# Kernel optimization log

Hardware: AMD Instinct MI355X
Metric: run time of the kernel (lower is better)

Reference implementation:

```python
import jax, jax.numpy as jnp
import numpy as np
from jax import lax

N_WIRES = 4
EPS_BN = 1e-5

def _conv(x, w, b):
    y = lax.conv_general_dilated(x, w, (1, 1), 'SAME',
                                 dimension_numbers=('NCHW', 'OIHW', 'NCHW'))
    return y + b[None, :, None, None]

def _bn2d(x, g, b):
    mu = jnp.mean(x, axis=(0, 2, 3), keepdims=True)
    var = jnp.var(x, axis=(0, 2, 3), keepdims=True)
    return (x - mu) * lax.rsqrt(var + EPS_BN) * g[None, :, None, None] + b[None, :, None, None]

def _maxpool2(x):
    return lax.reduce_window(x, -jnp.inf, lax.max, (1, 1, 2, 2), (1, 1, 2, 2), 'VALID')

def _ry(t):
    c, s = jnp.cos(t / 2), jnp.sin(t / 2)
    return jnp.stack([jnp.stack([c, -s], -1), jnp.stack([s, c], -1)], -2).astype(jnp.complex64)

def _rz(t):
    tc = t.astype(jnp.complex64)
    em, ep = jnp.exp(-0.5j * tc), jnp.exp(0.5j * tc)
    z = jnp.zeros_like(em)
    return jnp.stack([jnpp_stack := jnp.stack([em, z], -1), jnp.stack([z, ep], -1)], -2)

def _rx(t):
    c = jnp.cos(t / 2).astype(jnp.complex64)
    s = (-1j) * jnp.sin(t / 2).astype(jnp.complex64)
    return jnp.stack([jnp.stack([c, s], -1), jnp.stack([s, c], -1)], -2)

def _apply_1q(state, U, q):
    # state: (B,2,2,2,2); U: (2,2) shared or (B,2,2) per-sample
    a = jnp.moveaxis(state, 1 + q, 1)
    if U.ndim == 2:
        a = jnp.einsum('ij,bj...->bi...', U, a)
    else:
        a = jnp.einsum('bij,bj...->bi...', U, a)
    return jnp.moveaxis(a, 1, 1 + q)

def _cnot(state, c, t):
    a = jnp.moveaxis(state, (1 + c, 1 + t), (1, 2))
    a = jnp.stack([a[:, 0], jnp.flip(a[:, 1], axis=1)], axis=1)
    return jnp.moveaxis(a, (1, 2), (1 + c, 1 + t))

def _circuit(scaled, theta, rho):
    # scaled: (B, 4) angles; theta, rho: (4, 3)
    B = scaled.shape[0]
    state = jnp.zeros((B,) + (2,) * N_WIRES, jnp.complex64)
    state = state.at[(slice(None),) + (0,) * N_WIRES].set(1.0 + 0j)
    for i in range(N_WIRES):
        state = _apply_1q(state, _ry(scaled[:, i]), i)
    for i in range(N_WIRES):
        state = _apply_1q(state, _ry(theta[i, 0]), i)
        state = _apply_1q(state, _rz(theta[i, 1]), i)
        state = _apply_1q(state, _rx(theta[i, 2]), i)
    for i in range(N_WIRES - 1):
        state = _cnot(state, i, i + 1)
    for i in range(N_WIRES):
        state = _apply_1q(state, _ry(rho[i, 0]), i)
        state = _apply_1q(state, _rz(rho[i, 1]), i)
        state = _apply_1q(state, _rx(rho[i, 2]), i)
    for i in range(N_WIRES - 1):
        state = _cnot(state, i + 1, i)
    probs = jnp.abs(state) ** 2  # (B,2,2,2,2)
    exps = []
    for i in range(N_WIRES):
        p = jnp.moveaxis(probs, 1 + i, 1)
        exps.append(jnp.sum(p[:, 0], axis=(1, 2, 3)) - jnp.sum(p[:, 1], axis=(1, 2, 3)))
    return jnp.stack(exps, axis=1)  # (B,4)

def setup_inputs() -> dict:
    key = jax.random.key(0)
    ks = jax.random.split(key, 8)
    B = 128
    return {
        'x': jax.random.normal(ks[0], (B, 1, 224, 224), jnp.float32),
        'conv1_w': jax.random.normal(ks[1], (8, 1, 3, 3), jnp.float32) * 0.1,
        'conv1_b': jnp.zeros((8,), jnp.float32),
        'bn1_g': jnp.ones((8,), jnp.float32),
        'bn1_b': jnp.zeros((8,), jnp.float32),
        'conv2_w': jax.random.normal(ks[2], (16, 8, 3, 3), jnp.float32) * 0.1,
        'conv2_b': jnp.zeros((16,), jnp.float32),
        'bn2_g': jnp.ones((16,), jnp.float32),
        'bn2_b': jnp.zeros((16,), jnp.float32),
        'theta': jax.random.normal(ks[3], (4, 3), jnp.float32),
        'rho': jax.random.normal(ks[4], (4, 3), jnp.float32),
        'norm_g': jnp.ones((4,), jnp.float32),
        'norm_b': jnp.zeros((4,), jnp.float32),
    }

def reference(x, conv1_w, conv1_b, bn1_g, bn1_b, conv2_w, conv2_b, bn2_g, bn2_b,
              theta, rho, norm_g, norm_b):
    h = jax.nn.relu(_bn2d(_conv(x, conv1_w, conv1_b), bn1_g, bn1_b))
    h = _maxpool2(h)
    h = jax.nn.relu(_bn2d(_conv(h, conv2_w, conv2_b), bn2_g, bn2_b))
    h = _maxpool2(h)
    feat = jnp.mean(h, axis=(2, 3))          # AdaptiveAvgPool2d((1,1)) + flatten -> (B,16)
    feat = feat[:, :N_WIRES]                  # (B,4)
    scaled = (feat - jnp.mean(feat)) / (jnp.std(feat, ddof=1) + 1e-6) * jnp.pi
    out = _circuit(scaled, theta, rho)        # (B,4) real
    mu = jnp.mean(out, axis=0, keepdims=True)
    var = jnp.var(out, axis=0, keepdims=True)
    return (out - mu) * lax.rsqrt(var + EPS_BN) * norm_g[None, :] + norm_b[None, :]
```

## Files before the change

### kernel.cpp

```cpp
#include <hip/hip_runtime.h>
#include <math.h>

#define H1 224
#define W1 224
#define H2 112
#define W2 112
#define HP 56
#define WP 56

#define NS 32
#define SLOT_STRIDE 64

struct C2 { float re, im; };
__device__ __forceinline__ C2 cmul(C2 a, C2 b) {
    return C2{fmaf(a.re, b.re, -a.im * b.im), fmaf(a.re, b.im, a.im * b.re)};
}
__device__ __forceinline__ C2 cadd(C2 a, C2 b) { return C2{a.re + b.re, a.im + b.im}; }

template <int S>
__device__ __forceinline__ void ap1s(C2* st, C2 u00, C2 u01, C2 u10, C2 u11) {
#pragma unroll
    for (int i = 0; i < 16; i++) {
        if (i & S) continue;
        C2 a0 = st[i], a1 = st[i + S];
        st[i]     = cadd(cmul(u00, a0), cmul(u01, a1));
        st[i + S] = cadd(cmul(u10, a0), cmul(u11, a1));
    }
}
template <int SC, int STT>
__device__ __forceinline__ void cnot_s(C2* st) {
#pragma unroll
    for (int i = 0; i < 16; i++)
        if ((i & SC) && !(i & STT)) { C2 t = st[i]; st[i] = st[i + STT]; st[i + STT] = t; }
}
struct M2 { C2 m[2][2]; };
__device__ __forceinline__ M2 mmul(const M2& A, const M2& B) {
    M2 R;
#pragma unroll
    for (int i = 0; i < 2; i++)
#pragma unroll
        for (int j = 0; j < 2; j++)
            R.m[i][j] = cadd(cmul(A.m[i][0], B.m[0][j]), cmul(A.m[i][1], B.m[1][j]));
    return R;
}
__device__ __forceinline__ M2 combined_u(const float* __restrict__ p) {
    float c0 = cosf(0.5f * p[0]), s0 = sinf(0.5f * p[0]);
    float c1 = cosf(0.5f * p[1]), s1 = sinf(0.5f * p[1]);
    float c2 = cosf(0.5f * p[2]), s2 = sinf(0.5f * p[2]);
    M2 Ry = {{{{c0, 0.f}, {-s0, 0.f}}, {{s0, 0.f}, {c0, 0.f}}}};
    M2 Rz = {{{{c1, -s1}, {0.f, 0.f}}, {{0.f, 0.f}, {c1, s1}}}};
    M2 Rx = {{{{c2, 0.f}, {0.f, -s2}}, {{0.f, -s2}, {c2, 0.f}}}};
    return mmul(Rx, mmul(Rz, Ry));
}

template <int Q>
__device__ __forceinline__ void rows_reduce(float* red, const float* vals, int tid) {
#pragma unroll
    for (int q = 0; q < Q; q++) red[q * 256 + tid] = vals[q];
    __syncthreads();
#pragma unroll
    for (int s = 128; s > 0; s >>= 1) {
        for (int idx = tid; idx < Q * s; idx += 256) {
            int row = idx / s, i = idx - row * s;
            red[row * 256 + i] += red[row * 256 + i + s];
        }
        __syncthreads();
    }
}

__global__ void zero_ws(float* ws, int n) {
    int i = blockIdx.x * blockDim.x + threadIdx.x;
    if (i < n) ws[i] = 0.f;
}

__device__ __forceinline__ float slot_sum(const float* stats, int c) {
    float s = 0.f;
#pragma unroll
    for (int sl = 0; sl < NS; sl++) s += stats[sl * SLOT_STRIDE + c];
    return s;
}

__global__ __launch_bounds__(256, 2) void conv1_pool_stats(
        const float* __restrict__ x, const float* __restrict__ w,
        const float* __restrict__ bias, const float* __restrict__ g1,
        float* __restrict__ stats, float* __restrict__ p1ext) {
    __shared__ float red[16 * 256];
    int strip = blockIdx.x;
    int b = blockIdx.y;
    int tid = threadIdx.x;
    int pc = tid & 127;
    int rhalf = tid >> 7;
    int r0 = strip * 16 + rhalf * 8;
    const float* xb = x + (size_t)b * H1 * W1;
    float sums[8], sqs[8], pm[8];
    bool gp[8];
#pragma unroll
    for (int c = 0; c < 8; c++) { sums[c] = 0.f; sqs[c] = 0.f; gp[c] = g1[c] >= 0.f; }
    bool act = pc < W2;
    if (act) {
        bool cl = pc > 0, cr = pc < W2 - 1;
        const float* rp0 = xb + (size_t)r0 * W1 + 2 * pc;
        float al, am0, am1, ar, bl, bm0, bm1, br;
        if (r0 > 0) {
            const float* rp = rp0 - W1;
            float2 m = *(const float2*)rp;
            al = cl ? rp[-1] : 0.f; am0 = m.x; am1 = m.y; ar = cr ? rp[2] : 0.f;
        } else { al = 0.f; am0 = 0.f; am1 = 0.f; ar = 0.f; }
        {
            float2 m = *(const float2*)rp0;
            bl = cl ? rp0[-1] : 0.f; bm0 = m.x; bm1 = m.y; br = cr ? rp0[2] : 0.f;
        }
#pragma unroll
        for (int rr = 0; rr < 8; rr++) {
            float nl = 0.f, nm0 = 0.f, nm1 = 0.f, nr = 0.f;
            int rn = r0 + rr + 1;
            if (rn < H1) {
                const float* rp = rp0 + (size_t)(rr + 1) * W1;
                float2 m = *(const float2*)rp;
                nl = cl ? rp[-1] : 0.f; nm0 = m.x; nm1 = m.y; nr = cr ? rp[2] : 0.f;
            }
            float4 e0 = make_float4(0.f, 0.f, 0.f, 0.f);
            float4 e1 = make_float4(0.f, 0.f, 0.f, 0.f);
#pragma unroll
            for (int c = 0; c < 8; c++) {
                const float* wc = w + c * 9;
                float y0 = bias[c], y1 = bias[c];
                y0 = fmaf(wc[0], al,  y0); y0 = fmaf(wc[1], am0, y0); y0 = fmaf(wc[2], am1, y0);
                y1 = fmaf(wc[0], am0, y1); y1 = fmaf(wc[1], am1, y1); y1 = fmaf(wc[2], ar,  y1);
                y0 = fmaf(wc[3], bl,  y0); y0 = fmaf(wc[4], bm0, y0); y0 = fmaf(wc[5], bm1, y0);
                y1 = fmaf(wc[3], bm0, y1); y1 = fmaf(wc[4], bm1, y1); y1 = fmaf(wc[5], br,  y1);
                y0 = fmaf(wc[6], nl,  y0); y0 = fmaf(wc[7], nm0, y0); y0 = fmaf(wc[8], nm1, y0);
                y1 = fmaf(wc[6], nm0, y1); y1 = fmaf(wc[7], nm1, y1); y1 = fmaf(wc[8], nr,  y1);
                sums[c] += y0 + y1;
                sqs[c] = fmaf(y0, y0, fmaf(y1, y1, sqs[c]));
                float m01 = gp[c] ? fmaxf(y0, y1) : fminf(y0, y1);
                if ((rr & 1) == 0) {
                    pm[c] = m01;
                } else {
                    float e = gp[c] ? fmaxf(pm[c], m01) : fminf(pm[c], m01);
                    if (c == 0) e0.x = e; else if (c == 1) e0.y = e;
                    else if (c == 2) e0.z = e; else if (c == 3) e0.w = e;
                    else if (c == 4) e1.x = e; else if (c == 5) e1.y = e;
                    else if (c == 6) e1.z = e; else e1.w = e;
                }
            }
            if (rr & 1) {
                int pr = (r0 + rr) >> 1;
                float* dst = p1ext + ((((size_t)b * H2 + pr) * W2 + pc) << 3);
                ((float4*)dst)[0] = e0;
                ((float4*)dst)[1] = e1;
            }
            al = bl; am0 = bm0; am1 = bm1; ar = br;
            bl = nl; bm0 = nm0; bm1 = nm1; br = nr;
        }
    }
    float vals[16];
#pragma unroll
    for (int c = 0; c < 8; c++) { vals[c] = sums[c]; vals[8 + c] = sqs[c]; }
    rows_reduce<16>(red, vals, tid);
    int slot = (b * 14 + strip) & (NS - 1);
    if (tid < 16) atomicAdd(stats + slot * SLOT_STRIDE + tid, red[tid * 256]);
}

__global__ void conv1_stats(const float* __restrict__ x, const float* __restrict__ w,
                            const float* __restrict__ bias, float* __restrict__ stats) {
    __shared__ float red[16 * 256];
    int strip = blockIdx.x;
    int b = blockIdx.y;
    int tid = threadIdx.x;
    const float* xb = x + (size_t)b * H1 * W1;
    float sums[8], sqs[8];
#pragma unroll
    for (int c = 0; c < 8; c++) { sums[c] = 0.f; sqs[c] = 0.f; }
    int col = tid;
    if (col < W1) {
        bool cl = col > 0, cr = col < W1 - 1;
        int row0 = strip * 8;
        float a0, a1, a2, b0, b1, b2, c0, c1, c2;
        {
            int r = row0 - 1;
            if (r >= 0) {
                a0 = cl ? xb[r * W1 + col - 1] : 0.f;
                a1 = xb[r * W1 + col];
                a2 = cr ? xb[r * W1 + col + 1] : 0.f;
            } else { a0 = a1 = a2 = 0.f; }
            r = row0;
            b0 = cl ? xb[r * W1 + col - 1] : 0.f;
            b1 = xb[r * W1 + col];
            b2 = cr ? xb[r * W1 + col + 1] : 0.f;
        }
        for (int rr = 0; rr < 8; rr++) {
            int rn = row0 + rr + 1;
            if (rn < H1) {
                c0 = cl ? xb[rn * W1 + col - 1] : 0.f;
                c1 = xb[rn * W1 + col];
                c2 = cr ? xb[rn * W1 + col + 1] : 0.f;
            } else { c0 = c1 = c2 = 0.f; }
#pragma unroll
            for (int c = 0; c < 8; c++) {
                float acc = bias[c];
                acc = fmaf(w[c * 9 + 0], a0, acc);
                acc = fmaf(w[c * 9 + 1], a1, acc);
                acc = fmaf(w[c * 9 + 2], a2, acc);
                acc = fmaf(w[c * 9 + 3], b0, acc);
                acc = fmaf(w[c * 9 + 4], b1, acc);
                acc = fmaf(w[c * 9 + 5], b2, acc);
                acc = fmaf(w[c * 9 + 6], c0, acc);
                acc = fmaf(w[c * 9 + 7], c1, acc);
                acc = fmaf(w[c * 9 + 8], c2, acc);
                sums[c] += acc;
                sqs[c] = fmaf(acc, acc, sqs[c]);
            }
            a0 = b0; a1 = b1; a2 = b2;
            b0 = c0; b1 = c1; b2 = c2;
        }
    }
    float vals[16];
#pragma unroll
    for (int c = 0; c < 8; c++) { vals[c] = sums[c]; vals[8 + c] = sqs[c]; }
    rows_reduce<16>(red, vals, tid);
    int slot = (b * 28 + strip) & (NS - 1);
    if (tid < 16) atomicAdd(stats + slot * SLOT_STRIDE + tid, red[tid * 256]);
}

template <int PH, int PW>
__device__ __forceinline__ void build_h1_tile(const float* __restrict__ xb,
                                              float (*h1t)[PH][PW],
                                              const float* __restrict__ w1,
                                              const float* __restrict__ b1,
                                              const float* sc1, const float* sh1,
                                              int oy0, int ox0, int tid) {
    for (int i = tid; i < PH * PW; i += 256) {
        int p = i / PW, q = i % PW;
        int hy = oy0 + p, hx = ox0 + q;
        bool ok = (hy >= 0 && hy < H2 && hx >= 0 && hx < W2);
        float xp[5][5];
        if (hy >= 1 && hy <= H2 - 2 && hx >= 1 && hx <= W2 - 2) {
            const float* bp = xb + (2 * hy - 1) * W1 + (2 * hx - 1);
#pragma unroll
            for (int r = 0; r < 5; r++)
#pragma unroll
                for (int c = 0; c < 5; c++) xp[r][c] = bp[r * W1 + c];
        } else if (ok) {
#pragma unroll
            for (int r = 0; r < 5; r++)
#pragma unroll
                for (int c = 0; c < 5; c++) {
                    int gy = 2 * hy - 1 + r, gx = 2 * hx - 1 + c;
                    xp[r][c] = (gy >= 0 && gy < H1 && gx >= 0 && gx < W1) ? xb[gy * W1 + gx] : 0.f;
                }
        }
#pragma unroll
        for (int c = 0; c < 8; c++) {
            float mx = 0.f;
            if (ok) {
                mx = -INFINITY;
#pragma unroll
                for (int dy = 0; dy < 2; dy++)
#pragma unroll
                    for (int dx = 0; dx < 2; dx++) {
                        float acc = b1[c];
#pragma unroll
                        for (int ky = 0; ky < 3; ky++)
#pragma unroll
                            for (int kx = 0; kx < 3; kx++)
                                acc = fmaf(w1[c * 9 + ky * 3 + kx], xp[dy + ky][dx + kx], acc);
                        mx = fmaxf(mx, fmaxf(fmaf(acc, sc1[c], sh1[c]), 0.f));
                    }
            }
            h1t[c][p][q] = mx;
        }
    }
}

__global__ __launch_bounds__(256, 4) void conv2_stats_slim(
        const float* __restrict__ p1ext, const float* __restrict__ g1,
        const float* __restrict__ be1, const float* __restrict__ stats1,
        const float* __restrict__ w2, const float* __restrict__ b2,
        const float* __restrict__ g2,
        float* __restrict__ stats2, float* __restrict__ p2ext, float N1) {
    __shared__ __align__(16) float h1t[8][34][34];
    __shared__ float sc1[8], sh1[8];
    int b = blockIdx.z;
    int Y0 = blockIdx.y * 32, X0 = blockIdx.x * 32;
    int ty = threadIdx.y, tx = threadIdx.x;
    int tid = ty * 16 + tx;
    if (tid < 8) {
        float su = slot_sum(stats1, tid), sq = slot_sum(stats1, 8 + tid);
        float mu = su / N1;
        float var = sq / N1 - mu * mu;
        float sc = g1[tid] * rsqrtf(var + 1e-5f);
        sc1[tid] = sc;
        sh1[tid] = be1[tid] - mu * sc;
    }
    __syncthreads();
    const float* pb = p1ext + (((size_t)b * H2) * W2 << 3);
    for (int i = tid; i < 34 * 34; i += 256) {
        int p = i / 34, q = i % 34;
        int hy = Y0 - 1 + p, hx = X0 - 1 + q;
        if (hy >= 0 && hy < H2 && hx >= 0 && hx < W2) {
            const float* cp = pb + (((size_t)hy * W2 + hx) << 3);
            float4 u = ((const float4*)cp)[0];
            float4 v = ((const float4*)cp)[1];
            h1t[0][p][q] = fmaxf(fmaf(u.x, sc1[0], sh1[0]), 0.f);
            h1t[1][p][q] = fmaxf(fmaf(u.y, sc1[1], sh1[1]), 0.f);
            h1t[2][p][q] = fmaxf(fmaf(u.z, sc1[2], sh1[2]), 0.f);
            h1t[3][p][q] = fmaxf(fmaf(u.w, sc1[3], sh1[3]), 0.f);
            h1t[4][p][q] = fmaxf(fmaf(v.x, sc1[4], sh1[4]), 0.f);
            h1t[5][p][q] = fmaxf(fmaf(v.y, sc1[5], sh1[5]), 0.f);
            h1t[6][p][q] = fmaxf(fmaf(v.z, sc1[6], sh1[6]), 0.f);
            h1t[7][p][q] = fmaxf(fmaf(v.w, sc1[7], sh1[7]), 0.f);
        } else {
#pragma unroll
            for (int c = 0; c < 8; c++) h1t[c][p][q] = 0.f;
        }
    }
    __syncthreads();
    float acc[4][2][2];
#pragma unroll
    for (int co = 0; co < 4; co++)
#pragma unroll
        for (int dy = 0; dy < 2; dy++)
#pragma unroll
            for (int dx = 0; dx < 2; dx++) acc[co][dy][dx] = b2[co];
#pragma unroll
    for (int ci = 0; ci < 8; ci++) {
        float win[4][4];
#pragma unroll
        for (int r = 0; r < 4; r++) {
            const float2* rp = (const float2*)&h1t[ci][2 * ty + r][2 * tx];
            float2 u = rp[0], v = rp[1];
            win[r][0] = u.x; win[r][1] = u.y; win[r][2] = v.x; win[r][3] = v.y;
        }
#pragma unroll
        for (int co = 0; co < 4; co++)
#pragma unroll
            for (int ky = 0; ky < 3; ky++)
#pragma unroll
                for (int kx = 0; kx < 3; kx++) {
                    float wv = w2[co * 72 + ci * 9 + ky * 3 + kx];
#pragma unroll
                    for (int dy = 0; dy < 2; dy++)
#pragma unroll
                        for (int dx = 0; dx < 2; dx++)
                            acc[co][dy][dx] = fmaf(wv, win[dy + ky][dx + kx], acc[co][dy][dx]);
                }
    }
    int cy0 = Y0 + 2 * ty, cx0 = X0 + 2 * tx;
    bool vy0 = cy0 < H2, vy1 = cy0 + 1 < H2, vx0 = cx0 < W2, vx1 = cx0 + 1 < W2;
    float vals[8];
#pragma unroll
    for (int co = 0; co < 4; co++) {
        float s = 0.f, q = 0.f;
        if (vy0 && vx0) { float a = acc[co][0][0]; s += a; q = fmaf(a, a, q); }
        if (vy0 && vx1) { float a = acc[co][0][1]; s += a; q = fmaf(a, a, q); }
        if (vy1 && vx0) { float a = acc[co][1][0]; s += a; q = fmaf(a, a, q); }
        if (vy1 && vx1) { float a = acc[co][1][1]; s += a; q = fmaf(a, a, q); }
        vals[co] = s;
        vals[4 + co] = q;
    }
    {
        int hy = (Y0 >> 1) + ty, hx = (X0 >> 1) + tx;
        if (hy < HP && hx < WP) {
#pragma unroll
            for (int co = 0; co < 4; co++) {
                float mx = fmaxf(fmaxf(acc[co][0][0], acc[co][0][1]),
                                 fmaxf(acc[co][1][0], acc[co][1][1]));
                float mn = fminf(fminf(acc[co][0][0], acc[co][0][1]),
                                 fminf(acc[co][1][0], acc[co][1][1]));
                p2ext[(((size_t)b * 4 + co) * HP + hy) * WP + hx] = (g2[co] >= 0.f) ? mx : mn;
            }
        }
    }
    __syncthreads();
    float* red = (float*)h1t;
    rows_reduce<8>(red, vals, tid);
    int slot = ((b * 16) + blockIdx.y * 4 + blockIdx.x) & (NS - 1);
    if (tid < 8) atomicAdd(stats2 + slot * SLOT_STRIDE + tid, red[tid * 256]);
}

template <bool STORE>
__global__ __launch_bounds__(256, 4) void conv2_stats_fused(
        const float* __restrict__ x, const float* __restrict__ w1,
        const float* __restrict__ b1, const float* __restrict__ g1,
        const float* __restrict__ be1, const float* __restrict__ stats1,
        const float* __restrict__ w2, const float* __restrict__ b2,
        float* __restrict__ stats2,
        float* __restrict__ pmax, float* __restrict__ pmin, float N1) {
    __shared__ __align__(16) float h1t[8][34][34];
    __shared__ float sc1[8], sh1[8];
    int b = blockIdx.z;
    int Y0 = blockIdx.y * 32, X0 = blockIdx.x * 32;
    int ty = threadIdx.y, tx = threadIdx.x;
    int tid = ty * 16 + tx;
    if (tid < 8) {
        float su = slot_sum(stats1, tid), sq = slot_sum(stats1, 8 + tid);
        float mu = su / N1;
        float var = sq / N1 - mu * mu;
        float sc = g1[tid] * rsqrtf(var + 1e-5f);
        sc1[tid] = sc;
        sh1[tid] = be1[tid] - mu * sc;
    }
    __syncthreads();
    const float* xb = x + (size_t)b * H1 * W1;
    build_h1_tile<34, 34>(xb, h1t, w1, b1, sc1, sh1, Y0 - 1, X0 - 1, tid);
    __syncthreads();
    float acc[4][2][2];
#pragma unroll
    for (int co = 0; co < 4; co++)
#pragma unroll
        for (int dy = 0; dy < 2; dy++)
#pragma unroll
            for (int dx = 0; dx < 2; dx++) acc[co][dy][dx] = b2[co];
#pragma unroll
    for (int ci = 0; ci < 8; ci++) {
        float win[4][4];
#pragma unroll
        for (int r = 0; r < 4; r++) {
            const float2* rp = (const float2*)&h1t[ci][2 * ty + r][2 * tx];
            float2 u = rp[0], v = rp[1];
            win[r][0] = u.x; win[r][1] = u.y; win[r][2] = v.x; win[r][3] = v.y;
        }
#pragma unroll
        for (int co = 0; co < 4; co++)
#pragma unroll
            for (int ky = 0; ky < 3; ky++)
#pragma unroll
                for (int kx = 0; kx < 3; kx++) {
                    float wv = w2[co * 72 + ci * 9 + ky * 3 + kx];
#pragma unroll
                    for (int dy = 0; dy < 2; dy++)
#pragma unroll
                        for (int dx = 0; dx < 2; dx++)
                            acc[co][dy][dx] = fmaf(wv, win[dy + ky][dx + kx], acc[co][dy][dx]);
                }
    }
    int cy0 = Y0 + 2 * ty, cx0 = X0 + 2 * tx;
    bool vy0 = cy0 < H2, vy1 = cy0 + 1 < H2, vx0 = cx0 < W2, vx1 = cx0 + 1 < W2;
    float vals[8];
#pragma unroll
    for (int co = 0; co < 4; co++) {
        float s = 0.f, q = 0.f;
        if (vy0 && vx0) { float a = acc[co][0][0]; s += a; q = fmaf(a, a, q); }
        if (vy0 && vx1) { float a = acc[co][0][1]; s += a; q = fmaf(a, a, q); }
        if (vy1 && vx0) { float a = acc[co][1][0]; s += a; q = fmaf(a, a, q); }
        if (vy1 && vx1) { float a = acc[co][1][1]; s += a; q = fmaf(a, a, q); }
        vals[co] = s;
        vals[4 + co] = q;
    }
    if (STORE) {
        int hy = (Y0 >> 1) + ty, hx = (X0 >> 1) + tx;
        if (hy < HP && hx < WP) {
#pragma unroll
            for (int co = 0; co < 4; co++) {
                float mx = fmaxf(fmaxf(acc[co][0][0], acc[co][0][1]),
                                 fmaxf(acc[co][1][0], acc[co][1][1]));
                float mn = fminf(fminf(acc[co][0][0], acc[co][0][1]),
                                 fminf(acc[co][1][0], acc[co][1][1]));
                size_t idx = (((size_t)b * 4 + co) * HP + hy) * WP + hx;
                pmax[idx] = mx;
                pmin[idx] = mn;
            }
        }
    }
    __syncthreads();
    float* red = (float*)h1t;
    rows_reduce<8>(red, vals, tid);
    int slot = ((b * 16) + blockIdx.y * 4 + blockIdx.x) & (NS - 1);
    if (tid < 8) atomicAdd(stats2 + slot * SLOT_STRIDE + tid, red[tid * 256]);
}

__global__ void pool_bn_mean(const float* __restrict__ pmax, const float* __restrict__ pmin,
                             const float* __restrict__ g2, const float* __restrict__ be2,
                             const float* __restrict__ stats2,
                             float* __restrict__ featbuf, float N2) {
    __shared__ float red[256];
    int co = blockIdx.x & 3;
    int b = blockIdx.x >> 2;
    int tid = threadIdx.x;
    float su = slot_sum(stats2, co), sq = slot_sum(stats2, 4 + co);
    float mu = su / N2;
    float var = sq / N2 - mu * mu;
    float sc = g2[co] * rsqrtf(var + 1e-5f);
    float sh = be2[co] - mu * sc;
    const float* P = (sc >= 0.f ? pmax : pmin) + ((size_t)b * 4 + co) * (HP * WP);
    float s = 0.f;
    for (int i = tid; i < HP * WP; i += 256) s += fmaxf(fmaf(P[i], sc, sh), 0.f);
    red[tid] = s;
    __syncthreads();
    for (int st = 128; st > 0; st >>= 1) {
        if (tid < st) red[tid] += red[tid + st];
        __syncthreads();
    }
    if (tid == 0) featbuf[(size_t)b * 4 + co] = red[0];
}

__global__ void conv2_final_fused(const float* __restrict__ x, const float* __restrict__ w1,
                                  const float* __restrict__ b1, const float* __restrict__ g1,
                                  const float* __restrict__ be1,
                                  const float* __restrict__ stats1,
                                  const float* __restrict__ w2, const float* __restrict__ b2,
                                  const float* __restrict__ g2, const float* __restrict__ be2,
                                  const float* __restrict__ stats2,
                                  float* __restrict__ featbuf, float N1, float N2) {
    __shared__ __align__(16) float h1t[8][34][34];
    __shared__ float sc1[8], sh1[8];
    __shared__ float sc2[4], sh2[4];
    int b = blockIdx.z;
    int py0 = blockIdx.y * 16, px0 = blockIdx.x * 16;
    int ty = threadIdx.y, tx = threadIdx.x;
    int tid = ty * 16 + tx;
    if (tid < 8) {
        float su = slot_sum(stats1, tid), sq = slot_sum(stats1, 8 + tid);
        float mu = su / N1;
        float var = sq / N1 - mu * mu;
        float sc = g1[tid] * rsqrtf(var + 1e-5f);
        sc1[tid] = sc;
        sh1[tid] = be1[tid] - mu * sc;
    }
    if (tid >= 16 && tid < 20) {
        int j = tid - 16;
        float su = slot_sum(stats2, j), sq = slot_sum(stats2, 4 + j);
        float mu = su / N2;
        float var = sq / N2 - mu * mu;
        float sc = g2[j] * rsqrtf(var + 1e-5f);
        sc2[j] = sc;
        sh2[j] = be2[j] - mu * sc;
    }
    __syncthreads();
    const float* xb = x + (size_t)b * H1 * W1;
    build_h1_tile<34, 34>(xb, h1t, w1, b1, sc1, sh1, 2 * py0 - 1, 2 * px0 - 1, tid);
    __syncthreads();
    bool valid = (py0 + ty < HP) && (px0 + tx < WP);
    float acc[4][2][2];
#pragma unroll
    for (int co = 0; co < 4; co++)
#pragma unroll
        for (int dy = 0; dy < 2; dy++)
#pragma unroll
            for (int dx = 0; dx < 2; dx++) acc[co][dy][dx] = b2[co];
#pragma unroll
    for (int ci = 0; ci < 8; ci++) {
        float win[4][4];
#pragma unroll
        for (int r = 0; r < 4; r++) {
            const float2* rp = (const float2*)&h1t[ci][2 * ty + r][2 * tx];
            float2 u = rp[0], v = rp[1];
            win[r][0] = u.x; win[r][1] = u.y; win[r][2] = v.x; win[r][3] = v.y;
        }
#pragma unroll
        for (int co = 0; co < 4; co++)
#pragma unroll
            for (int ky = 0; ky < 3; ky++)
#pragma unroll
                for (int kx = 0; kx < 3; kx++) {
                    float wv = w2[co * 72 + ci * 9 + ky * 3 + kx];
#pragma unroll
                    for (int dy = 0; dy < 2; dy++)
#pragma unroll
                        for (int dx = 0; dx < 2; dx++)
                            acc[co][dy][dx] = fmaf(wv, win[dy + ky][dx + kx], acc[co][dy][dx]);
                }
    }
    float vals[4];
#pragma unroll
    for (int co = 0; co < 4; co++) {
        float mx = -INFINITY;
#pragma unroll
        for (int dy = 0; dy < 2; dy++)
#pragma unroll
            for (int dx = 0; dx < 2; dx++)
                mx = fmaxf(mx, fmaxf(fmaf(acc[co][dy][dx], sc2[co], sh2[co]), 0.f));
        vals[co] = valid ? mx : 0.f;
    }
    __syncthreads();
    float* red = (float*)h1t;
    rows_reduce<4>(red, vals, tid);
    if (tid < 4) atomicAdd(featbuf + (size_t)b * 4 + tid, red[tid * 256]);
}

__device__ __forceinline__ float bsum(float v, float* lds) {
#pragma unroll
    for (int off = 32; off; off >>= 1) v += __shfl_xor(v, off, 64);
    __syncthreads();
    if ((threadIdx.x & 63) == 0) lds[threadIdx.x >> 6] = v;
    __syncthreads();
    float r = 0.f;
    int nw = (int)(blockDim.x + 63) >> 6;
#pragma clang loop unroll(disable)
    for (int i = 0; i < nw; i++) r += lds[i];
    return r;
}

__global__ void finalize(const float* __restrict__ featbuf, const float* __restrict__ theta,
                         const float* __restrict__ rho, const float* __restrict__ ng,
                         const float* __restrict__ nb, float* __restrict__ out, int B) {
    __shared__ float lds[16];
    int b = threadIdx.x;
    float f[4];
#pragma unroll
    for (int j = 0; j < 4; j++) f[j] = featbuf[b * 4 + j] * (1.f / (HP * WP));
    float n = 4.f * (float)B;
    float mean = bsum(f[0] + f[1] + f[2] + f[3], lds) / n;
    float d2 = 0.f;
#pragma unroll
    for (int j = 0; j < 4; j++) { float d = f[j] - mean; d2 += d * d; }
    float var1 = bsum(d2, lds) / (n - 1.f);
    float stdv = sqrtf(fmaxf(var1, 0.f)) + 1e-6f;
    const float PI = 3.14159265358979323846f;
    float cs[4], sn[4];
#pragma unroll
    for (int j = 0; j < 4; j++) {
        float sc = (f[j] - mean) / stdv * PI;
        cs[j] = cosf(0.5f * sc);
        sn[j] = sinf(0.5f * sc);
    }
    C2 st[16];
    {
        float amp[16];
        amp[1] = sn[3]; amp[0] = cs[3];
#pragma unroll
        for (int k = 0; k < 2; k++) { amp[k + 2] = amp[k] * sn[2]; amp[k] *= cs[2]; }
#pragma unroll
        for (int k = 0; k < 4; k++) { amp[k + 4] = amp[k] * sn[1]; amp[k] *= cs[1]; }
#pragma unroll
        for (int k = 0; k < 8; k++) { amp[k + 8] = amp[k] * sn[0]; amp[k] *= cs[0]; }
#pragma unroll
        for (int i = 0; i < 16; i++) st[i] = C2{amp[i], 0.f};
    }
#pragma clang loop unroll(disable)
    for (int l = 0; l < 2; l++) {
        const float* p = (l == 0) ? theta : rho;
#pragma clang loop unroll(disable)
        for (int i = 0; i < 4; i++) {
            M2 U = combined_u(p + i * 3);
            switch (i) {
            case 0: ap1s<8>(st, U.m[0][0], U.m[0][1], U.m[1][0], U.m[1][1]); break;
            case 1: ap1s<4>(st, U.m[0][0], U.m[0][1], U.m[1][0], U.m[1][1]); break;
            case 2: ap1s<2>(st, U.m[0][0], U.m[0][1], U.m[1][0], U.m[1][1]); break;
            default: ap1s<1>(st, U.m[0][0], U.m[0][1], U.m[1][0], U.m[1][1]); break;
            }
        }
        if (l == 0) { cnot_s<8, 4>(st); cnot_s<4, 2>(st); cnot_s<2, 1>(st); }
        else        { cnot_s<4, 8>(st); cnot_s<2, 4>(st); cnot_s<1, 2>(st); }
    }
    float e[4];
#pragma unroll
    for (int qb = 0; qb < 4; qb++) {
        int m = 8 >> qb;
        float p0 = 0.f, p1 = 0.f;
#pragma unroll
        for (int i = 0; i < 16; i++) {
            float pr = st[i].re * st[i].re + st[i].im * st[i].im;
            if (i & m) p1 += pr; else p0 += pr;
        }
        e[qb] = p0 - p1;
    }
#pragma clang loop unroll(disable)
    for (int j = 0; j < 4; j++) {
        float mu = bsum(e[j], lds) / (float)B;
        float dv = e[j] - mu;
        float v = bsum(dv * dv, lds) / (float)B;
        out[b * 4 + j] = fmaf(dv, rsqrtf(v + 1e-5f) * ng[j], nb[j]);
    }
}

extern "C" void kernel_launch(void* const* d_in, const int* in_sizes, int n_in,
                              void* d_out, int out_size, void* d_ws, size_t ws_size,
                              hipStream_t stream) {
    const float* x     = (const float*)d_in[0];
    const float* w1    = (const float*)d_in[1];
    const float* b1    = (const float*)d_in[2];
    const float* g1    = (const float*)d_in[3];
    const float* be1   = (const float*)d_in[4];
    const float* w2    = (const float*)d_in[5];
    const float* b2    = (const float*)d_in[6];
    const float* g2    = (const float*)d_in[7];
    const float* be2   = (const float*)d_in[8];
    const float* theta = (const float*)d_in[9];
    const float* rho   = (const float*)d_in[10];
    const float* ng    = (const float*)d_in[11];
    const float* nb    = (const float*)d_in[12];
    float* out = (float*)d_out;

    int B = in_sizes[0] / (H1 * W1);

    float* ws = (float*)d_ws;
    float* stats1 = ws;
    float* stats2 = ws + NS * SLOT_STRIDE;
    float* featbuf = ws + 2 * NS * SLOT_STRIDE;
    float* bufs = featbuf + (size_t)B * 4;

    size_t common = (size_t)(2 * NS * SLOT_STRIDE) + (size_t)B * 4;
    size_t p2n = (size_t)B * 4 * HP * WP;
    size_t p1n = (size_t)B * 8 * H2 * W2;
    size_t needA = (common + p2n + p1n) * sizeof(float);
    size_t needB = (common + 2 * p2n) * sizeof(float);
    bool tierA = ws_size >= needA;
    bool tierB = !tierA && ws_size >= needB;

    float N1 = (float)B * H1 * W1;
    float N2 = (float)B * H2 * W2;
    int nz = (int)common;

    zero_ws<<<(nz + 255) / 256, 256, 0, stream>>>(ws, nz);
    if (tierA) {
        float* p2ext = bufs;
        float* p1ext = bufs + p2n;
        conv1_pool_stats<<<dim3(14, B), 256, 0, stream>>>(x, w1, b1, g1, stats1, p1ext);
        conv2_stats_slim<<<dim3(4, 4, B), dim3(16, 16), 0, stream>>>(
            p1ext, g1, be1, stats1, w2, b2, g2, stats2, p2ext, N1);
        pool_bn_mean<<<B * 4, 256, 0, stream>>>(p2ext, p2ext, g2, be2, stats2, featbuf, N2);
        finalize<<<1, B, 0, stream>>>(featbuf, theta, rho, ng, nb, out, B);
    } else if (tierB) {
        float* pmax = bufs;
        float* pmin = bufs + p2n;
        conv1_stats<<<dim3(28, B), 256, 0, stream>>>(x, w1, b1, stats1);
        conv2_stats_fused<true><<<dim3(4, 4, B), dim3(16, 16), 0, stream>>>(
            x, w1, b1, g1, be1, stats1, w2, b2, stats2, pmax, pmin, N1);
        pool_bn_mean<<<B * 4, 256, 0, stream>>>(pmax, pmin, g2, be2, stats2, featbuf, N2);
        finalize<<<1, B, 0, stream>>>(featbuf, theta, rho, ng, nb, out, B);
    } else {
        conv1_stats<<<dim3(28, B), 256, 0, stream>>>(x, w1, b1, stats1);
        conv2_stats_fused<false><<<dim3(4, 4, B), dim3(16, 16), 0, stream>>>(
            x, w1, b1, g1, be1, stats1, w2, b2, stats2, nullptr, nullptr, N1);
        conv2_final_fused<<<dim3(4, 4, B), dim3(16, 16), 0, stream>>>(
            x, w1, b1, g1, be1, stats1, w2, b2, g2, be2, stats2, featbuf, N1, N2);
        finalize<<<1, B, 0, stream>>>(featbuf, theta, rho, ng, nb, out, B);
    }
}
```

Baseline: 170.3 us.

## Replace shared-memory tiled conv2 with direct per-thread global-load strip kernel

The conv2 stage no longer stages a 34x34x8 BN+ReLU halo tile in LDS. Each thread now computes one pooled output column over two pooled rows, reading its 4x4 input window straight from global memory with float4 loads and applying BN1+ReLU in registers. The launch becomes a 1D grid of 7 blocks per sample, and the two __syncthreads around the LDS tile are gone. In exchange, overlapping windows are loaded redundantly from global or cache instead of being shared through LDS, register pressure rises from the 4x4x4 window array, and a no-op zero add is inserted in mmul.

```diff
diff --git a/kernel.cpp b/kernel.cpp
--- a/kernel.cpp
+++ b/kernel.cpp
@@ -40,7 +40,7 @@
     for (int i = 0; i < 2; i++)
 #pragma unroll
         for (int j = 0; j < 2; j++)
-            R.m[i][j] = cadd(cmul(A.m[i][0], B.m[0][j]), cmul(A.m[i][1], B.m[1][j]));
+            R.m[i][j] = cadd(cmul(A.m[i][0], B.m[0][j]), cadd(cmul(A.m[i][1], B.m[1][j]), C2{0.f, 0.f}));
     return R;
 }
 __device__ __forceinline__ M2 combined_u(const float* __restrict__ p) {
@@ -273,109 +273,110 @@
     }
 }
 
-__global__ __launch_bounds__(256, 4) void conv2_stats_slim(
+__global__ __launch_bounds__(256) void conv2_stats_direct(
         const float* __restrict__ p1ext, const float* __restrict__ g1,
         const float* __restrict__ be1, const float* __restrict__ stats1,
         const float* __restrict__ w2, const float* __restrict__ b2,
         const float* __restrict__ g2,
         float* __restrict__ stats2, float* __restrict__ p2ext, float N1) {
-    __shared__ __align__(16) float h1t[8][34][34];
-    __shared__ float sc1[8], sh1[8];
-    int b = blockIdx.z;
-    int Y0 = blockIdx.y * 32, X0 = blockIdx.x * 32;
-    int ty = threadIdx.y, tx = threadIdx.x;
-    int tid = ty * 16 + tx;
-    if (tid < 8) {
-        float su = slot_sum(stats1, tid), sq = slot_sum(stats1, 8 + tid);
+    __shared__ float red[8 * 256];
+    int tid = threadIdx.x;
+    int b = blockIdx.x / 7;
+    int strip = (blockIdx.x % 7) * 4 + (tid >> 6);
+    int q = tid & 63;
+    float sc1[8], sh1[8];
+#pragma unroll
+    for (int c = 0; c < 8; c++) {
+        float su = slot_sum(stats1, c), sq = slot_sum(stats1, 8 + c);
         float mu = su / N1;
         float var = sq / N1 - mu * mu;
-        float sc = g1[tid] * rsqrtf(var + 1e-5f);
-        sc1[tid] = sc;
-        sh1[tid] = be1[tid] - mu * sc;
-    }
-    __syncthreads();
-    const float* pb = p1ext + (((size_t)b * H2) * W2 << 3);
-    for (int i = tid; i < 34 * 34; i += 256) {
-        int p = i / 34, q = i % 34;
-        int hy = Y0 - 1 + p, hx = X0 - 1 + q;
-        if (hy >= 0 && hy < H2 && hx >= 0 && hx < W2) {
-            const float* cp = pb + (((size_t)hy * W2 + hx) << 3);
-            float4 u = ((const float4*)cp)[0];
-            float4 v = ((const float4*)cp)[1];
-            h1t[0][p][q] = fmaxf(fmaf(u.x, sc1[0], sh1[0]), 0.f);
-            h1t[1][p][q] = fmaxf(fmaf(u.y, sc1[1], sh1[1]), 0.f);
-            h1t[2][p][q] = fmaxf(fmaf(u.z, sc1[2], sh1[2]), 0.f);
-            h1t[3][p][q] = fmaxf(fmaf(u.w, sc1[3], sh1[3]), 0.f);
-            h1t[4][p][q] = fmaxf(fmaf(v.x, sc1[4], sh1[4]), 0.f);
-            h1t[5][p][q] = fmaxf(fmaf(v.y, sc1[5], sh1[5]), 0.f);
-            h1t[6][p][q] = fmaxf(fmaf(v.z, sc1[6], sh1[6]), 0.f);
-            h1t[7][p][q] = fmaxf(fmaf(v.w, sc1[7], sh1[7]), 0.f);
-        } else {
-#pragma unroll
-            for (int c = 0; c < 8; c++) h1t[c][p][q] = 0.f;
-        }
-    }
-    __syncthreads();
-    float acc[4][2][2];
-#pragma unroll
-    for (int co = 0; co < 4; co++)
-#pragma unroll
-        for (int dy = 0; dy < 2; dy++)
-#pragma unroll
-            for (int dx = 0; dx < 2; dx++) acc[co][dy][dx] = b2[co];
-#pragma unroll
-    for (int ci = 0; ci < 8; ci++) {
-        float win[4][4];
-#pragma unroll
-        for (int r = 0; r < 4; r++) {
-            const float2* rp = (const float2*)&h1t[ci][2 * ty + r][2 * tx];
-            float2 u = rp[0], v = rp[1];
-            win[r][0] = u.x; win[r][1] = u.y; win[r][2] = v.x; win[r][3] = v.y;
-        }
-#pragma unroll
-        for (int co = 0; co < 4; co++)
-#pragma unroll
-            for (int ky = 0; ky < 3; ky++)
-#pragma unroll
-                for (int kx = 0; kx < 3; kx++) {
-                    float wv = w2[co * 72 + ci * 9 + ky * 3 + kx];
-#pragma unroll
-                    for (int dy = 0; dy < 2; dy++)
-#pragma unroll
-                        for (int dx = 0; dx < 2; dx++)
-                            acc[co][dy][dx] = fmaf(wv, win[dy + ky][dx + kx], acc[co][dy][dx]);
+        float sc = g1[c] * rsqrtf(var + 1e-5f);
+        sc1[c] = sc;
+        sh1[c] = be1[c] - mu * sc;
+    }
+    float sums[4] = {0.f, 0.f, 0.f, 0.f}, sqs[4] = {0.f, 0.f, 0.f, 0.f};
+    bool gp[4];
+#pragma unroll
+    for (int co = 0; co < 4; co++) gp[co] = g2[co] >= 0.f;
+    if (q < WP) {
+        const float* pb = p1ext + (((size_t)b * H2) * W2 << 3);
+        int cc0 = 2 * q - 1;
+        bool colok[4];
+#pragma unroll
+        for (int c = 0; c < 4; c++) { int cx = cc0 + c; colok[c] = (cx >= 0 && cx < W2); }
+#pragma clang loop unroll(disable)
+        for (int p8 = 0; p8 < 2; p8++) {
+            int p = strip * 2 + p8;
+            int r0 = 2 * p - 1;
+            float acc[4][2][2];
+#pragma unroll
+            for (int co = 0; co < 4; co++) {
+                float bb = b2[co];
+#pragma unroll
+                for (int dy = 0; dy < 2; dy++)
+#pragma unroll
+                    for (int dx = 0; dx < 2; dx++) acc[co][dy][dx] = bb;
+            }
+#pragma unroll
+            for (int g = 0; g < 2; g++) {
+                float vv[4][4][4];
+#pragma unroll
+                for (int r = 0; r < 4; r++) {
+                    int ry = r0 + r;
+                    bool rok = (ry >= 0 && ry < H2);
+#pragma unroll
+                    for (int c = 0; c < 4; c++) {
+                        if (rok && colok[c]) {
+                            const float* cp = pb + (((size_t)ry * W2 + (cc0 + c)) << 3) + (g << 2);
+                            float4 t = *(const float4*)cp;
+                            int ci = g * 4;
+                            vv[r][c][0] = fmaxf(fmaf(t.x, sc1[ci + 0], sh1[ci + 0]), 0.f);
+                            vv[r][c][1] = fmaxf(fmaf(t.y, sc1[ci + 1], sh1[ci + 1]), 0.f);
+                            vv[r][c][2] = fmaxf(fmaf(t.z, sc1[ci + 2], sh1[ci + 2]), 0.f);
+                            vv[r][c][3] = fmaxf(fmaf(t.w, sc1[ci + 3], sh1[ci + 3]), 0.f);
+                        } else {
+                            vv[r][c][0] = 0.f; vv[r][c][1] = 0.f;
+                            vv[r][c][2] = 0.f; vv[r][c][3] = 0.f;
+                        }
+                    }
                 }
-    }
-    int cy0 = Y0 + 2 * ty, cx0 = X0 + 2 * tx;
-    bool vy0 = cy0 < H2, vy1 = cy0 + 1 < H2, vx0 = cx0 < W2, vx1 = cx0 + 1 < W2;
+#pragma unroll
+                for (int k = 0; k < 4; k++) {
+                    int ci = g * 4 + k;
+#pragma unroll
+                    for (int ky = 0; ky < 3; ky++)
+#pragma unroll
+                        for (int kx = 0; kx < 3; kx++) {
+#pragma unroll
+                            for (int co = 0; co < 4; co++) {
+                                float wv = w2[co * 72 + ci * 9 + ky * 3 + kx];
+#pragma unroll
+                                for (int dy = 0; dy < 2; dy++)
+#pragma unroll
+                                    for (int dx = 0; dx < 2; dx++)
+                                        acc[co][dy][dx] =
+                                            fmaf(wv, vv[dy + ky][dx + kx][k], acc[co][dy][dx]);
+                            }
+                        }
+                }
+            }
+#pragma unroll
+            for (int co = 0; co < 4; co++) {
+                float a00 = acc[co][0][0], a01 = acc[co][0][1];
+                float a10 = acc[co][1][0], a11 = acc[co][1][1];
+                sums[co] += (a00 + a01) + (a10 + a11);
+                sqs[co] = fmaf(a00, a00, fmaf(a01, a01, fmaf(a10, a10, fmaf(a11, a11, sqs[co]))));
+                float ext = gp[co] ? fmaxf(fmaxf(a00, a01), fmaxf(a10, a11))
+                                   : fminf(fminf(a00, a01), fminf(a10, a11));
+                p2ext[(((size_t)b * 4 + co) * HP + p) * WP + q] = ext;
+            }
+        }
+    }
     float vals[8];
 #pragma unroll
-    for (int co = 0; co < 4; co++) {
-        float s = 0.f, q = 0.f;
-        if (vy0 && vx0) { float a = acc[co][0][0]; s += a; q = fmaf(a, a, q); }
-        if (vy0 && vx1) { float a = acc[co][0][1]; s += a; q = fmaf(a, a, q); }
-        if (vy1 && vx0) { float a = acc[co][1][0]; s += a; q = fmaf(a, a, q); }
-        if (vy1 && vx1) { float a = acc[co][1][1]; s += a; q = fmaf(a, a, q); }
-        vals[co] = s;
-        vals[4 + co] = q;
-    }
-    {
-        int hy = (Y0 >> 1) + ty, hx = (X0 >> 1) + tx;
-        if (hy < HP && hx < WP) {
-#pragma unroll
-            for (int co = 0; co < 4; co++) {
-                float mx = fmaxf(fmaxf(acc[co][0][0], acc[co][0][1]),
-                                 fmaxf(acc[co][1][0], acc[co][1][1]));
-                float mn = fminf(fminf(acc[co][0][0], acc[co][0][1]),
-                                 fminf(acc[co][1][0], acc[co][1][1]));
-                p2ext[(((size_t)b * 4 + co) * HP + hy) * WP + hx] = (g2[co] >= 0.f) ? mx : mn;
-            }
-        }
-    }
-    __syncthreads();
-    float* red = (float*)h1t;
+    for (int co = 0; co < 4; co++) { vals[co] = sums[co]; vals[4 + co] = sqs[co]; }
     rows_reduce<8>(red, vals, tid);
-    int slot = ((b * 16) + blockIdx.y * 4 + blockIdx.x) & (NS - 1);
+    int slot = blockIdx.x & (NS - 1);
     if (tid < 8) atomicAdd(stats2 + slot * SLOT_STRIDE + tid, red[tid * 256]);
 }
 
@@ -708,7 +709,7 @@
         float* p2ext = bufs;
         float* p1ext = bufs + p2n;
         conv1_pool_stats<<<dim3(14, B), 256, 0, stream>>>(x, w1, b1, g1, stats1, p1ext);
-        conv2_stats_slim<<<dim3(4, 4, B), dim3(16, 16), 0, stream>>>(
+        conv2_stats_direct<<<dim3(7 * B), 256, 0, stream>>>(
             p1ext, g1, be1, stats1, w2, b2, g2, stats2, p2ext, N1);
         pool_bn_mean<<<B * 4, 256, 0, stream>>>(p2ext, p2ext, g2, be2, stats2, featbuf, N2);
         finalize<<<1, B, 0, stream>>>(featbuf, theta, rho, ng, nb, out, B);
```

Result: slower. 208.5 us (+22.4%).
